# Optimization experiments

Measured on AMD Instinct MI355X. Metric: run time of the kernel, lower is better.

## Reference

```python
import jax, jax.numpy as jnp
import numpy as np

A = 0.4          # sigma: uniform noise half-width Uniform(-A, A)
THRESHOLD = 1.0
TAU_INV = 0.5    # module stores 1.0 / tau with tau = 2.0


@jax.custom_vjp
def spike(v, unif):
    # StochasticST.forward: bernoulli(clamp((v + A) / (2A), 0, 1))
    p = jnp.clip((v + A) / (2.0 * A), 0.0, 1.0)
    return (unif < p).astype(v.dtype)


def _spike_fwd(v, unif):
    return spike(v, unif), v


def _spike_bwd(v, g):
    # StochasticST.backward: straight-through window [-A, A] with slope 1/(2A)
    surrogate = ((v >= -A) & (v <= A)).astype(g.dtype) * (1.0 / (2.0 * A))
    return (g * surrogate, jnp.zeros(v.shape, g.dtype))


spike.defvjp(_spike_fwd, _spike_bwd)


def setup_inputs() -> dict:
    key = jax.random.key(0)
    k1, k2, k3 = jax.random.split(key, 3)
    B, T, N = 32, 16, 65536
    x = jax.random.normal(k1, (B, T, N), dtype=jnp.float32)
    # pre-sampled uniform_(-A, A) noise (one draw per timestep/element)
    noise = jax.random.uniform(k2, (B, T, N), dtype=jnp.float32, minval=-A, maxval=A)
    # pre-sampled uniforms driving the bernoulli spike draw
    unif = jax.random.uniform(k3, (B, T, N), dtype=jnp.float32)
    return {"x": x, "noise": noise, "unif": unif}


def reference(x, noise, unif):
    # x: [B, T, N] -> scan over T with membrane state u: [B, N]
    xt = jnp.swapaxes(x, 0, 1)      # [T, B, N]
    nt = jnp.swapaxes(noise, 0, 1)  # [T, B, N]
    rt = jnp.swapaxes(unif, 0, 1)   # [T, B, N]
    u0 = jnp.zeros((x.shape[0], x.shape[2]), x.dtype)

    def step(u, inp):
        xi, ni, ri = inp
        u = TAU_INV * u + xi          # leaky integrate
        u = u - ni                    # u += -Uniform(-A, A) noise injection
        o = spike(u - THRESHOLD, ri)  # stochastic threshold spike
        u = u * (1.0 - o)             # hard reset where spiked
        return u, o

    _, o = jax.lax.scan(step, u0, (xt, nt, rt))
    return jnp.swapaxes(o, 0, 1)  # [B, T, N] spike train
```

## Files before the change

### kernel.cpp

```cpp
#include <hip/hip_runtime.h>


namespace {

constexpr int B = 32;
constexpr int T = 16;
constexpr int N = 65536;
constexpr int N4 = N / 4;
constexpr int N4_SHIFT = 14;
constexpr int HALF = (B / 2) * T * N4;

constexpr float SIGMA = 0.4f;
constexpr float TWO_SIGMA = 0.8f;
constexpr float THRESHOLD = 1.0f;
constexpr float TAU_INV = 0.5f;

__device__ __forceinline__ float lif_step(float& u, float xi, float ni, float ri) {
    u = TAU_INV * u + xi;
    u = u - ni;
    float v = u - THRESHOLD;
    float p = (v + SIGMA) / TWO_SIGMA;
    p = fminf(fmaxf(p, 0.0f), 1.0f);
    float o = (ri < p) ? 1.0f : 0.0f;
    u = u * (1.0f - o);
    return o;
}

__device__ __forceinline__ float4 lif_step4(float4& u, const float4& xi,
                                            const float4& ni, const float4& ri) {
    float4 o;
    o.x = lif_step(u.x, xi.x, ni.x, ri.x);
    o.y = lif_step(u.y, xi.y, ni.y, ri.y);
    o.z = lif_step(u.z, xi.z, ni.z, ri.z);
    o.w = lif_step(u.w, xi.w, ni.w, ri.w);
    return o;
}

__global__ __launch_bounds__(256) void snn_scan_kernel(
    const float4* __restrict__ x,
    const float4* __restrict__ noise,
    const float4* __restrict__ unif,
    float4* __restrict__ out)
{
    const int tid = blockIdx.x * blockDim.x + threadIdx.x;
    const int b0 = tid >> N4_SHIFT;
    const int nc = tid & (N4 - 1);

    int idx0 = b0 * T * N4 + nc;
    int idx1 = idx0 + HALF;

    float4 u0 = make_float4(0.f, 0.f, 0.f, 0.f);
    float4 u1 = make_float4(0.f, 0.f, 0.f, 0.f);

    float4 cx0 = x[idx0], cn0 = noise[idx0], cr0 = unif[idx0];
    float4 cx1 = x[idx1], cn1 = noise[idx1], cr1 = unif[idx1];

    for (int t = 0; t < T - 1; ++t) {
        const int nidx0 = idx0 + N4;
        const int nidx1 = idx1 + N4;
        float4 nx0 = x[nidx0], nn0 = noise[nidx0], nr0 = unif[nidx0];
        float4 nx1 = x[nidx1], nn1 = noise[nidx1], nr1 = unif[nidx1];

        out[idx0] = lif_step4(u0, cx0, cn0, cr0);
        out[idx1] = lif_step4(u1, cx1, cn1, cr1);

        cx0 = nx0; cn0 = nn0; cr0 = nr0;
        cx1 = nx1; cn1 = nn1; cr1 = nr1;
        idx0 = nidx0; idx1 = nidx1;
    }

    out[idx0] = lif_step4(u0, cx0, cn0, cr0);
    out[idx1] = lif_step4(u1, cx1, cn1, cr1);
}

}

extern "C" void kernel_launch(void* const* d_in, const int* in_sizes, int n_in,
                              void* d_out, int out_size, void* d_ws, size_t ws_size,
                              hipStream_t stream) {
    const float4* x     = (const float4*)d_in[0];
    const float4* noise = (const float4*)d_in[1];
    const float4* unif  = (const float4*)d_in[2];
    float4* out         = (float4*)d_out;

    const int threads_total = (B / 2) * N4;
    const int block = 256;
    const int grid = threads_total / block;

    snn_scan_kernel<<<grid, block, 0, stream>>>(x, noise, unif, out);
}
```

Baseline: 393.9 us.

## Use one batch row per thread with non-temporal output stores

```diff
diff --git a/kernel.cpp b/kernel.cpp
--- a/kernel.cpp
+++ b/kernel.cpp
@@ -8,12 +8,13 @@
 constexpr int N = 65536;
 constexpr int N4 = N / 4;
 constexpr int N4_SHIFT = 14;
-constexpr int HALF = (B / 2) * T * N4;
 
 constexpr float SIGMA = 0.4f;
 constexpr float TWO_SIGMA = 0.8f;
 constexpr float THRESHOLD = 1.0f;
 constexpr float TAU_INV = 0.5f;
+
+typedef float floatv4 __attribute__((ext_vector_type(4)));
 
 __device__ __forceinline__ float lif_step(float& u, float xi, float ni, float ri) {
     u = TAU_INV * u + xi;
@@ -36,6 +37,10 @@
     return o;
 }
 
+__device__ __forceinline__ void store_nt(float4* p, const float4& v) {
+    __builtin_nontemporal_store(*(const floatv4*)&v, (floatv4*)p);
+}
+
 __global__ __launch_bounds__(256) void snn_scan_kernel(
     const float4* __restrict__ x,
     const float4* __restrict__ noise,
@@ -43,34 +48,29 @@
     float4* __restrict__ out)
 {
     const int tid = blockIdx.x * blockDim.x + threadIdx.x;
-    const int b0 = tid >> N4_SHIFT;
+    const int b = tid >> N4_SHIFT;
     const int nc = tid & (N4 - 1);
 
-    int idx0 = b0 * T * N4 + nc;
-    int idx1 = idx0 + HALF;
+    int idx = b * T * N4 + nc;
 
-    float4 u0 = make_float4(0.f, 0.f, 0.f, 0.f);
-    float4 u1 = make_float4(0.f, 0.f, 0.f, 0.f);
+    float4 u = make_float4(0.f, 0.f, 0.f, 0.f);
 
-    float4 cx0 = x[idx0], cn0 = noise[idx0], cr0 = unif[idx0];
-    float4 cx1 = x[idx1], cn1 = noise[idx1], cr1 = unif[idx1];
+    float4 cx = x[idx], cn = noise[idx], cr = unif[idx];
 
+    #pragma unroll 1
     for (int t = 0; t < T - 1; ++t) {
-        const int nidx0 = idx0 + N4;
-        const int nidx1 = idx1 + N4;
-        float4 nx0 = x[nidx0], nn0 = noise[nidx0], nr0 = unif[nidx0];
-        float4 nx1 = x[nidx1], nn1 = noise[nidx1], nr1 = unif[nidx1];
+        const int nidx = idx + N4;
+        float4 nx = x[nidx], nn = noise[nidx], nr = unif[nidx];
 
-        out[idx0] = lif_step4(u0, cx0, cn0, cr0);
-        out[idx1] = lif_step4(u1, cx1, cn1, cr1);
+        float4 o = lif_step4(u, cx, cn, cr);
+        store_nt(&out[idx], o);
 
-        cx0 = nx0; cn0 = nn0; cr0 = nr0;
-        cx1 = nx1; cn1 = nn1; cr1 = nr1;
-        idx0 = nidx0; idx1 = nidx1;
+        cx = nx; cn = nn; cr = nr;
+        idx = nidx;
     }
 
-    out[idx0] = lif_step4(u0, cx0, cn0, cr0);
-    out[idx1] = lif_step4(u1, cx1, cn1, cr1);
+    float4 o = lif_step4(u, cx, cn, cr);
+    store_nt(&out[idx], o);
 }
 
 }
@@ -83,7 +83,7 @@
     const float4* unif  = (const float4*)d_in[2];
     float4* out         = (float4*)d_out;
 
-    const int threads_total = (B / 2) * N4;
+    const int threads_total = B * N4;
     const int block = 256;
     const int grid = threads_total / block;
 
```

Measured after the change: 399.3 us. No clear change (+1.4%).
